# Kernel optimization log

Measured on AMD Instinct MI355X. Metric: run time of the kernel, lower is better.

Reference implementation:

```python
import jax, jax.numpy as jnp
import numpy as np

T, B, H = 2048, 32, 1024
L1, L2, L3 = 100, 10, 1  # cascade 100 -> 10 -> 1 from linear_size=100


def setup_inputs() -> dict:
    key = jax.random.key(0)
    ks = jax.random.split(key, 8)
    def lin_init(k, fan_in, shape):
        # torch nn.Linear default: U(-1/sqrt(fan_in), 1/sqrt(fan_in))
        bound = 1.0 / np.sqrt(fan_in)
        return jax.random.uniform(k, shape, jnp.float32, -bound, bound)
    return {
        "encoder_output": jax.random.normal(ks[0], (T, B, H), jnp.float32),
        "lengths": jax.random.randint(ks[1], (B,), 1, T + 1, jnp.int64),
        "W1": lin_init(ks[2], H, (L1, H)),
        "b1": lin_init(ks[3], H, (L1,)),
        "W2": lin_init(ks[4], L1, (L2, L1)),
        "b2": lin_init(ks[5], L1, (L2,)),
        "W3": lin_init(ks[6], L2, (L3, L2)),
        "b3": lin_init(ks[7], L2, (L3,)),
    }


def reference(encoder_output, lengths, W1, b1, W2, b2, W3, b3):
    # MLP cascade over all timesteps/batch at once: [T,B,H] -> [T,B,1]
    h = jax.nn.relu(jnp.einsum("tbh,lh->tbl", encoder_output, W1) + b1)
    h = jax.nn.relu(jnp.einsum("tbl,ml->tbm", h, W2) + b2)
    logits = jnp.einsum("tbm,om->tbo", h, W3) + b3  # [T,B,1]
    logp = jax.nn.log_sigmoid(logits)[..., 0]       # [T,B]
    # Mask timesteps beyond each sample's length, sum, exponentiate
    mask = jnp.arange(T)[:, None] < lengths[None, :]  # [T,B]
    return jnp.exp(jnp.sum(jnp.where(mask, logp, 0.0), axis=0))  # [B]
```

## Files before the change

kernel.cpp:

```cpp
#include <hip/hip_runtime.h>
#include <stdint.h>


#define T_DIM 2048
#define B_DIM 32
#define H_DIM 1024
#define L1_DIM 100
#define L1_PAD 112
#define L2_DIM 10
#define L2_PAD 16
#define K2_PAD 128
#define NBLK  1024

#define W1B_ELEMS (L1_PAD * H_DIM)
#define W2B_ELEMS (L2_PAD * K2_PAD)
#define PART_OFF_BYTES ((W1B_ELEMS + W2B_ELEMS) * 2)

typedef float v4f __attribute__((ext_vector_type(4)));
typedef short s8  __attribute__((ext_vector_type(8)));

static __device__ __forceinline__ unsigned short f2bf(float f) {
    unsigned int u = __float_as_uint(f);
    u += 0x7fffu + ((u >> 16) & 1u);
    return (unsigned short)(u >> 16);
}

__global__ void convert_weights(const float* __restrict__ W1,
                                const float* __restrict__ W2,
                                unsigned short* __restrict__ wsb) {
    int i = blockIdx.x * 256 + threadIdx.x;
    if (i < W1B_ELEMS) {
        int row = i >> 10, col = i & 1023;
        float v = (row < L1_DIM) ? W1[row * H_DIM + col] : 0.0f;
        wsb[i] = f2bf(v);
    } else {
        int j = i - W1B_ELEMS;
        if (j < W2B_ELEMS) {
            int r = j >> 7, c = j & 127;
            float v = (r < L2_DIM && c < L1_DIM) ? W2[r * L1_DIM + c] : 0.0f;
            wsb[W1B_ELEMS + j] = f2bf(v);
        }
    }
}

__global__ __launch_bounds__(256) void mlp_main(
    const float* __restrict__ enc,
    const int*   __restrict__ lenp,
    const float* __restrict__ b1,
    const float* __restrict__ b2,
    const float* __restrict__ W3,
    const float* __restrict__ b3,
    const unsigned short* __restrict__ w1b,
    const unsigned short* __restrict__ w2b,
    float* __restrict__ partials)
{
    __shared__ __align__(16) unsigned short ldsB[L1_PAD][72];
    __shared__ __align__(16) unsigned short ldsH[64][136];
    __shared__ __align__(16) unsigned short ldsW2[L2_PAD][136];
    __shared__ float ldsPart[2][32];

    const int tid  = threadIdx.x;
    const int blk  = blockIdx.x;
    const int lane = tid & 63;
    const int w    = tid >> 6;
    const int m    = lane & 15;
    const int q    = lane >> 4;

    const bool is64 = (lenp[1] == 0);

    const int tA = 2 * blk + (w >> 1);
    const int bA = ((w & 1) << 4) + m;
    const int lenA = is64 ? lenp[2 * bA] : lenp[bA];
    const bool predA = (tA < lenA);

    int maxlen = 0;
    for (int i = 0; i < B_DIM; ++i) {
        int L = is64 ? lenp[2 * i] : lenp[i];
        maxlen = max(maxlen, L);
    }
    if (2 * blk >= maxlen) {
        if (tid < 32) partials[tid * NBLK + blk] = 0.0f;
        return;
    }

    {
        int r = tid >> 4;
        int c = (tid & 15) << 3;
        *(uint4*)&ldsW2[r][c] = *(const uint4*)(w2b + r * K2_PAD + c);
    }

    float b1v[7];
#pragma unroll
    for (int nt = 0; nt < 7; ++nt) {
        int n = nt * 16 + m;
        b1v[nt] = (n < L1_DIM) ? b1[n] : 0.0f;
    }
    const float b2v = (m < L2_DIM) ? b2[m] : 0.0f;
    const float w3v = (m < L2_DIM) ? W3[m] : 0.0f;
    const float b3s = b3[0];

    const float* aptr = enc + (size_t)(blk * 64 + w * 16 + m) * H_DIM + q * 8;

    v4f acc[7];
#pragma unroll
    for (int nt = 0; nt < 7; ++nt) acc[nt] = (v4f)0.0f;

    for (int kc = 0; kc < 16; ++kc) {
        __syncthreads();
        {
            int base = tid;
#pragma unroll
            for (int it = 0; it < 4; ++it, base += 256) {
                if (it < 3 || base < 896) {
                    int r = base >> 3;
                    int c = (base & 7) << 3;
                    *(uint4*)&ldsB[r][c] =
                        *(const uint4*)(w1b + r * H_DIM + kc * 64 + c);
                }
            }
        }
        __syncthreads();
#pragma unroll
        for (int ks = 0; ks < 2; ++ks) {
            const int k0 = kc * 64 + ks * 32;
            float4 x0, x1;
            if (predA) {
                x0 = *(const float4*)(aptr + k0);
                x1 = *(const float4*)(aptr + k0 + 4);
            } else {
                x0 = make_float4(0.f, 0.f, 0.f, 0.f);
                x1 = make_float4(0.f, 0.f, 0.f, 0.f);
            }
            s8 afrag;
            afrag[0] = (short)f2bf(x0.x); afrag[1] = (short)f2bf(x0.y);
            afrag[2] = (short)f2bf(x0.z); afrag[3] = (short)f2bf(x0.w);
            afrag[4] = (short)f2bf(x1.x); afrag[5] = (short)f2bf(x1.y);
            afrag[6] = (short)f2bf(x1.z); afrag[7] = (short)f2bf(x1.w);
#pragma unroll
            for (int nt = 0; nt < 7; ++nt) {
                s8 bfrag = *(const s8*)&ldsB[nt * 16 + m][ks * 32 + q * 8];
                acc[nt] = __builtin_amdgcn_mfma_f32_16x16x32_bf16(
                    afrag, bfrag, acc[nt], 0, 0, 0);
            }
        }
    }

    __syncthreads();
#pragma unroll
    for (int nt = 0; nt < 7; ++nt) {
#pragma unroll
        for (int reg = 0; reg < 4; ++reg) {
            float h = fmaxf(acc[nt][reg] + b1v[nt], 0.0f);
            ldsH[w * 16 + q * 4 + reg][nt * 16 + m] = f2bf(h);
        }
    }
    {
        int r = tid >> 2;
        int c = 112 + ((tid & 3) << 2);
        *(uint2*)&ldsH[r][c] = make_uint2(0u, 0u);
    }
    __syncthreads();

    v4f acc2 = (v4f)0.0f;
#pragma unroll
    for (int ks = 0; ks < 4; ++ks) {
        s8 a2  = *(const s8*)&ldsH[w * 16 + m][ks * 32 + q * 8];
        s8 b2f = *(const s8*)&ldsW2[m][ks * 32 + q * 8];
        acc2 = __builtin_amdgcn_mfma_f32_16x16x32_bf16(a2, b2f, acc2, 0, 0, 0);
    }

    v4f z;
#pragma unroll
    for (int reg = 0; reg < 4; ++reg) {
        float y2 = fmaxf(acc2[reg] + b2v, 0.0f);
        z[reg] = y2 * w3v;
    }
#pragma unroll
    for (int msk = 1; msk < 16; msk <<= 1) {
#pragma unroll
        for (int reg = 0; reg < 4; ++reg)
            z[reg] += __shfl_xor(z[reg], msk, 16);
    }
    if (m == 0) {
#pragma unroll
        for (int reg = 0; reg < 4; ++reg) {
            int rowLocal = q * 4 + reg;
            int bC = ((w & 1) << 4) + rowLocal;
            int lenC = is64 ? lenp[2 * bC] : lenp[bC];
            float logit = z[reg] + b3s;
            float logp  = fminf(logit, 0.0f) - log1pf(__expf(-fabsf(logit)));
            ldsPart[w >> 1][bC] = (tA < lenC) ? logp : 0.0f;
        }
    }
    __syncthreads();
    if (tid < 32)
        partials[tid * NBLK + blk] = ldsPart[0][tid] + ldsPart[1][tid];
}

__global__ void finalize(const float* __restrict__ partials,
                         float* __restrict__ out) {
    const int b = blockIdx.x;
    const int tid = threadIdx.x;
    float s = 0.0f;
    for (int i = tid; i < NBLK; i += 256) s += partials[b * NBLK + i];
#pragma unroll
    for (int off = 32; off > 0; off >>= 1) s += __shfl_down(s, off, 64);
    __shared__ float red[4];
    if ((tid & 63) == 0) red[tid >> 6] = s;
    __syncthreads();
    if (tid == 0) out[b] = expf(red[0] + red[1] + red[2] + red[3]);
}

extern "C" void kernel_launch(void* const* d_in, const int* in_sizes, int n_in,
                              void* d_out, int out_size, void* d_ws, size_t ws_size,
                              hipStream_t stream) {
    const float* enc = (const float*)d_in[0];
    const int*   len = (const int*)d_in[1];
    const float* W1  = (const float*)d_in[2];
    const float* b1  = (const float*)d_in[3];
    const float* W2  = (const float*)d_in[4];
    const float* b2  = (const float*)d_in[5];
    const float* W3  = (const float*)d_in[6];
    const float* b3  = (const float*)d_in[7];

    unsigned short* wsb = (unsigned short*)d_ws;
    float* partials = (float*)((char*)d_ws + PART_OFF_BYTES);
    float* out = (float*)d_out;

    convert_weights<<<(W1B_ELEMS + W2B_ELEMS + 255) / 256, 256, 0, stream>>>(W1, W2, wsb);
    mlp_main<<<NBLK, 256, 0, stream>>>(enc, len, b1, b2, W3, b3,
                                       wsb, wsb + W1B_ELEMS, partials);
    finalize<<<B_DIM, 256, 0, stream>>>(partials, out);
}
```

Before: 375.5 us.

## Load W1 fragments directly from global and register-prefetch encoder tiles

```diff
diff --git a/kernel.cpp b/kernel.cpp
--- a/kernel.cpp
+++ b/kernel.cpp
@@ -8,12 +8,11 @@
 #define L1_DIM 100
 #define L1_PAD 112
 #define L2_DIM 10
-#define L2_PAD 16
 #define K2_PAD 128
 #define NBLK  1024
 
 #define W1B_ELEMS (L1_PAD * H_DIM)
-#define W2B_ELEMS (L2_PAD * K2_PAD)
+#define W2B_ELEMS (16 * K2_PAD)
 #define PART_OFF_BYTES ((W1B_ELEMS + W2B_ELEMS) * 2)
 
 typedef float v4f __attribute__((ext_vector_type(4)));
@@ -54,9 +53,8 @@
     const unsigned short* __restrict__ w2b,
     float* __restrict__ partials)
 {
-    __shared__ __align__(16) unsigned short ldsB[L1_PAD][72];
     __shared__ __align__(16) unsigned short ldsH[64][136];
-    __shared__ __align__(16) unsigned short ldsW2[L2_PAD][136];
+    __shared__ __align__(16) unsigned short ldsW2[16][136];
     __shared__ float ldsPart[2][32];
 
     const int tid  = threadIdx.x;
@@ -99,53 +97,54 @@
     const float w3v = (m < L2_DIM) ? W3[m] : 0.0f;
     const float b3s = b3[0];
 
-    const float* aptr = enc + (size_t)(blk * 64 + w * 16 + m) * H_DIM + q * 8;
+    const float* ap = enc + (size_t)(blk * 64 + w * 16 + m) * H_DIM + q * 8;
+    const unsigned short* wp = w1b + m * H_DIM + q * 8;
 
     v4f acc[7];
 #pragma unroll
     for (int nt = 0; nt < 7; ++nt) acc[nt] = (v4f)0.0f;
 
+#define LOADA(dst, off)                                                  \
+    do {                                                                 \
+        if (predA) dst = *(const float4*)(ap + (off));                   \
+        else       dst = make_float4(0.f, 0.f, 0.f, 0.f);                \
+    } while (0)
+
+    float4 aP0, aP1, aP2, aP3;
+    LOADA(aP0, 0); LOADA(aP1, 4); LOADA(aP2, 32); LOADA(aP3, 36);
+
+#pragma unroll 4
     for (int kc = 0; kc < 16; ++kc) {
-        __syncthreads();
-        {
-            int base = tid;
-#pragma unroll
-            for (int it = 0; it < 4; ++it, base += 256) {
-                if (it < 3 || base < 896) {
-                    int r = base >> 3;
-                    int c = (base & 7) << 3;
-                    *(uint4*)&ldsB[r][c] =
-                        *(const uint4*)(w1b + r * H_DIM + kc * 64 + c);
-                }
-            }
-        }
-        __syncthreads();
+        float4 aN0, aN1, aN2, aN3;
+        if (kc < 15) {
+            const int o = (kc + 1) * 64;
+            LOADA(aN0, o); LOADA(aN1, o + 4); LOADA(aN2, o + 32); LOADA(aN3, o + 36);
+        } else {
+            aN0 = aN1 = aN2 = aN3 = make_float4(0.f, 0.f, 0.f, 0.f);
+        }
 #pragma unroll
         for (int ks = 0; ks < 2; ++ks) {
-            const int k0 = kc * 64 + ks * 32;
-            float4 x0, x1;
-            if (predA) {
-                x0 = *(const float4*)(aptr + k0);
-                x1 = *(const float4*)(aptr + k0 + 4);
-            } else {
-                x0 = make_float4(0.f, 0.f, 0.f, 0.f);
-                x1 = make_float4(0.f, 0.f, 0.f, 0.f);
-            }
-            s8 afrag;
-            afrag[0] = (short)f2bf(x0.x); afrag[1] = (short)f2bf(x0.y);
-            afrag[2] = (short)f2bf(x0.z); afrag[3] = (short)f2bf(x0.w);
-            afrag[4] = (short)f2bf(x1.x); afrag[5] = (short)f2bf(x1.y);
-            afrag[6] = (short)f2bf(x1.z); afrag[7] = (short)f2bf(x1.w);
-#pragma unroll
-            for (int nt = 0; nt < 7; ++nt) {
-                s8 bfrag = *(const s8*)&ldsB[nt * 16 + m][ks * 32 + q * 8];
+            const unsigned short* wk = wp + kc * 64 + ks * 32;
+            s8 bfr[7];
+#pragma unroll
+            for (int nt = 0; nt < 7; ++nt)
+                bfr[nt] = *(const s8*)(wk + nt * 16 * H_DIM);
+            const float4 x0 = ks ? aP2 : aP0;
+            const float4 x1 = ks ? aP3 : aP1;
+            s8 af;
+            af[0] = (short)f2bf(x0.x); af[1] = (short)f2bf(x0.y);
+            af[2] = (short)f2bf(x0.z); af[3] = (short)f2bf(x0.w);
+            af[4] = (short)f2bf(x1.x); af[5] = (short)f2bf(x1.y);
+            af[6] = (short)f2bf(x1.z); af[7] = (short)f2bf(x1.w);
+#pragma unroll
+            for (int nt = 0; nt < 7; ++nt)
                 acc[nt] = __builtin_amdgcn_mfma_f32_16x16x32_bf16(
-                    afrag, bfrag, acc[nt], 0, 0, 0);
-            }
-        }
-    }
-
-    __syncthreads();
+                    af, bfr[nt], acc[nt], 0, 0, 0);
+        }
+        aP0 = aN0; aP1 = aN1; aP2 = aN2; aP3 = aN3;
+    }
+#undef LOADA
+
 #pragma unroll
     for (int nt = 0; nt < 7; ++nt) {
 #pragma unroll
```

New measurement: 430.1 us. +14.5%, slower.

## Double-buffer W1 tiles via direct global-to-LDS loads, two row tiles per wave

Applied to the files above, without the earlier changes.

```diff
diff --git a/kernel.cpp b/kernel.cpp
--- a/kernel.cpp
+++ b/kernel.cpp
@@ -1,4 +1,5 @@
 #include <hip/hip_runtime.h>
+#include <hip/hip_bf16.h>
 #include <stdint.h>
 
 
@@ -6,15 +7,19 @@
 #define B_DIM 32
 #define H_DIM 1024
 #define L1_DIM 100
-#define L1_PAD 112
 #define L2_DIM 10
-#define L2_PAD 16
 #define K2_PAD 128
-#define NBLK  1024
-
-#define W1B_ELEMS (L1_PAD * H_DIM)
-#define W2B_ELEMS (L2_PAD * K2_PAD)
+#define NPART 512
+
+#define W1B_ELEMS (112 * 1024)
+#define W2B_ELEMS (16 * 128)
 #define PART_OFF_BYTES ((W1B_ELEMS + W2B_ELEMS) * 2)
+
+#define CHUNK_BYTES 14336
+#define LDSH_OFF    0
+#define LDSW2_OFF   34816
+#define LDSPART_OFF 39168
+#define LDS_TOTAL   39680
 
 typedef float v4f __attribute__((ext_vector_type(4)));
 typedef short s8  __attribute__((ext_vector_type(8)));
@@ -23,6 +28,15 @@
     unsigned int u = __float_as_uint(f);
     u += 0x7fffu + ((u >> 16) & 1u);
     return (unsigned short)(u >> 16);
+}
+
+static __device__ __forceinline__ s8 pack8(float4 a, float4 b) {
+    union { s8 v; __hip_bfloat162 h[4]; } u;
+    u.h[0] = __float22bfloat162_rn(make_float2(a.x, a.y));
+    u.h[1] = __float22bfloat162_rn(make_float2(a.z, a.w));
+    u.h[2] = __float22bfloat162_rn(make_float2(b.x, b.y));
+    u.h[3] = __float22bfloat162_rn(make_float2(b.z, b.w));
+    return u.v;
 }
 
 __global__ void convert_weights(const float* __restrict__ W1,
@@ -54,10 +68,7 @@
     const unsigned short* __restrict__ w2b,
     float* __restrict__ partials)
 {
-    __shared__ __align__(16) unsigned short ldsB[L1_PAD][72];
-    __shared__ __align__(16) unsigned short ldsH[64][136];
-    __shared__ __align__(16) unsigned short ldsW2[L2_PAD][136];
-    __shared__ float ldsPart[2][32];
+    __shared__ __align__(16) unsigned char smem[LDS_TOTAL];
 
     const int tid  = threadIdx.x;
     const int blk  = blockIdx.x;
@@ -68,25 +79,27 @@
 
     const bool is64 = (lenp[1] == 0);
 
-    const int tA = 2 * blk + (w >> 1);
-    const int bA = ((w & 1) << 4) + m;
-    const int lenA = is64 ? lenp[2 * bA] : lenp[bA];
-    const bool predA = (tA < lenA);
-
     int maxlen = 0;
     for (int i = 0; i < B_DIM; ++i) {
         int L = is64 ? lenp[2 * i] : lenp[i];
         maxlen = max(maxlen, L);
     }
-    if (2 * blk >= maxlen) {
-        if (tid < 32) partials[tid * NBLK + blk] = 0.0f;
+    if (4 * blk >= maxlen) {
+        if (tid < 32) partials[tid * NPART + blk] = 0.0f;
         return;
     }
 
+    const int t = 4 * blk + w;
+    const int len0 = is64 ? lenp[2 * m] : lenp[m];
+    const int len1 = is64 ? lenp[2 * (16 + m)] : lenp[16 + m];
+    const bool pred0 = (t < len0);
+    const bool pred1 = (t < len1);
+    const bool waveActive = (t < maxlen);
+
     {
-        int r = tid >> 4;
-        int c = (tid & 15) << 3;
-        *(uint4*)&ldsW2[r][c] = *(const uint4*)(w2b + r * K2_PAD + c);
+        unsigned short* ldsW2 = (unsigned short*)(smem + LDSW2_OFF);
+        int r = tid >> 4, c = (tid & 15) << 3;
+        *(uint4*)(ldsW2 + r * 136 + c) = *(const uint4*)(w2b + r * K2_PAD + c);
     }
 
     float b1v[7];
@@ -99,102 +112,153 @@
     const float w3v = (m < L2_DIM) ? W3[m] : 0.0f;
     const float b3s = b3[0];
 
-    const float* aptr = enc + (size_t)(blk * 64 + w * 16 + m) * H_DIM + q * 8;
-
-    v4f acc[7];
-#pragma unroll
-    for (int nt = 0; nt < 7; ++nt) acc[nt] = (v4f)0.0f;
-
-    for (int kc = 0; kc < 16; ++kc) {
-        __syncthreads();
-        {
-            int base = tid;
-#pragma unroll
-            for (int it = 0; it < 4; ++it, base += 256) {
-                if (it < 3 || base < 896) {
-                    int r = base >> 3;
-                    int c = (base & 7) << 3;
-                    *(uint4*)&ldsB[r][c] =
-                        *(const uint4*)(w1b + r * H_DIM + kc * 64 + c);
-                }
+    const float* ap0 = enc + (size_t)(blk * 128 + w * 32 + m) * H_DIM + q * 8;
+    const float* ap1 = ap0 + 16 * H_DIM;
+    const int fragoff = lane * 16;
+
+    v4f acc0[7], acc1[7];
+#pragma unroll
+    for (int nt = 0; nt < 7; ++nt) { acc0[nt] = (v4f)0.0f; acc1[nt] = (v4f)0.0f; }
+
+#define STAGE(kc, BASE)                                                        \
+    {                                                                          \
+        _Pragma("unroll")                                                      \
+        for (int it = 0; it < 4; ++it) {                                       \
+            int j = it * 256 + tid;                                            \
+            if (it < 3 || tid < 128) {                                         \
+                int rest = j >> 6;                           \
+                int ks = (rest >= 7) ? 1 : 0;                                  \
+                int nt = rest - ks * 7;                                        \
+                const unsigned short* g = w1b + (nt * 16 + (j & 15)) * H_DIM + \
+                                          (kc) * 64 + ks * 32 + ((j >> 4) & 3) * 8; \
+                __builtin_amdgcn_global_load_lds(                              \
+                    (const __attribute__((address_space(1))) unsigned int*)g,  \
+                    (__attribute__((address_space(3))) unsigned int*)           \
+                        (smem + (BASE) + (j & ~63) * 16),                      \
+                    16, 0, 0);                                                 \
+            }                                                                  \
+        }                                                                      \
+    }
+
+#define KBODY(kc, RD, WR)                                                      \
+    {                                                                          \
+        if ((kc) < 15) STAGE((kc) + 1, WR);                                    \
+        if (waveActive) {                                                      \
+            const int kb = (kc) * 64;                                          \
+            const float4 z4 = make_float4(0.f, 0.f, 0.f, 0.f);                 \
+            float4 a00 = pred0 ? *(const float4*)(ap0 + kb)      : z4;         \
+            float4 a01 = pred0 ? *(const float4*)(ap0 + kb + 4)  : z4;         \
+            float4 a02 = pred0 ? *(const float4*)(ap0 + kb + 32) : z4;         \
+            float4 a03 = pred0 ? *(const float4*)(ap0 + kb + 36) : z4;         \
+            float4 a10 = pred1 ? *(const float4*)(ap1 + kb)      : z4;         \
+            float4 a11 = pred1 ? *(const float4*)(ap1 + kb + 4)  : z4;         \
+            float4 a12 = pred1 ? *(const float4*)(ap1 + kb + 32) : z4;         \
+            float4 a13 = pred1 ? *(const float4*)(ap1 + kb + 36) : z4;         \
+            s8 af0 = pack8(a00, a01);                                          \
+            s8 af1 = pack8(a10, a11);                                          \
+            _Pragma("unroll")                                                  \
+            for (int nt = 0; nt < 7; ++nt) {                                   \
+                s8 bf = *(const s8*)(smem + (RD) + nt * 1024 + fragoff);       \
+                acc0[nt] = __builtin_amdgcn_mfma_f32_16x16x32_bf16(af0, bf, acc0[nt], 0, 0, 0); \
+                acc1[nt] = __builtin_amdgcn_mfma_f32_16x16x32_bf16(af1, bf, acc1[nt], 0, 0, 0); \
+            }                                                                  \
+            af0 = pack8(a02, a03);                                             \
+            af1 = pack8(a12, a13);                                             \
+            _Pragma("unroll")                                                  \
+            for (int nt = 0; nt < 7; ++nt) {                                   \
+                s8 bf = *(const s8*)(smem + (RD) + (7 + nt) * 1024 + fragoff); \
+                acc0[nt] = __builtin_amdgcn_mfma_f32_16x16x32_bf16(af0, bf, acc0[nt], 0, 0, 0); \
+                acc1[nt] = __builtin_amdgcn_mfma_f32_16x16x32_bf16(af1, bf, acc1[nt], 0, 0, 0); \
+            }                                                                  \
+        }                                                                      \
+        __syncthreads();                                                       \
+    }
+
+    STAGE(0, 0)
+    __syncthreads();
+
+    KBODY(0, 0, CHUNK_BYTES)
+    KBODY(1, CHUNK_BYTES, 0)
+    KBODY(2, 0, CHUNK_BYTES)
+    KBODY(3, CHUNK_BYTES, 0)
+    KBODY(4, 0, CHUNK_BYTES)
+    KBODY(5, CHUNK_BYTES, 0)
+    KBODY(6, 0, CHUNK_BYTES)
+    KBODY(7, CHUNK_BYTES, 0)
+    KBODY(8, 0, CHUNK_BYTES)
+    KBODY(9, CHUNK_BYTES, 0)
+    KBODY(10, 0, CHUNK_BYTES)
+    KBODY(11, CHUNK_BYTES, 0)
+    KBODY(12, 0, CHUNK_BYTES)
+    KBODY(13, CHUNK_BYTES, 0)
+    KBODY(14, 0, CHUNK_BYTES)
+    KBODY(15, CHUNK_BYTES, 0)
+
+#undef KBODY
+#undef STAGE
+
+    unsigned short* ldsH = (unsigned short*)(smem + LDSH_OFF);
+#pragma unroll
+    for (int f = 0; f < 2; ++f) {
+#pragma unroll
+        for (int nt = 0; nt < 7; ++nt) {
+#pragma unroll
+            for (int reg = 0; reg < 4; ++reg) {
+                int row = w * 32 + f * 16 + q * 4 + reg;
+                int col = nt * 16 + m;
+                float a = f ? acc1[nt][reg] : acc0[nt][reg];
+                ldsH[row * 136 + col] = f2bf(fmaxf(a + b1v[nt], 0.0f));
             }
         }
-        __syncthreads();
-#pragma unroll
-        for (int ks = 0; ks < 2; ++ks) {
-            const int k0 = kc * 64 + ks * 32;
-            float4 x0, x1;
-            if (predA) {
-                x0 = *(const float4*)(aptr + k0);
-                x1 = *(const float4*)(aptr + k0 + 4);
-            } else {
-                x0 = make_float4(0.f, 0.f, 0.f, 0.f);
-                x1 = make_float4(0.f, 0.f, 0.f, 0.f);
+    }
+    {
+        int r = tid >> 1, c = 112 + (tid & 1) * 8;
+        uint4 z; z.x = z.y = z.z = z.w = 0u;
+        *(uint4*)(ldsH + r * 136 + c) = z;
+    }
+    __syncthreads();
+
+    unsigned short* ldsW2 = (unsigned short*)(smem + LDSW2_OFF);
+    v4f acc2[2];
+    acc2[0] = (v4f)0.0f; acc2[1] = (v4f)0.0f;
+#pragma unroll
+    for (int ks2 = 0; ks2 < 4; ++ks2) {
+        s8 bw = *(const s8*)(ldsW2 + m * 136 + ks2 * 32 + q * 8);
+#pragma unroll
+        for (int f = 0; f < 2; ++f) {
+            s8 ah = *(const s8*)(ldsH + (w * 32 + f * 16 + m) * 136 + ks2 * 32 + q * 8);
+            acc2[f] = __builtin_amdgcn_mfma_f32_16x16x32_bf16(ah, bw, acc2[f], 0, 0, 0);
+        }
+    }
+
+    float* ldsPart = (float*)(smem + LDSPART_OFF);
+#pragma unroll
+    for (int f = 0; f < 2; ++f) {
+        v4f zv;
+#pragma unroll
+        for (int reg = 0; reg < 4; ++reg)
+            zv[reg] = fmaxf(acc2[f][reg] + b2v, 0.0f) * w3v;
+#pragma unroll
+        for (int msk = 1; msk < 16; msk <<= 1) {
+#pragma unroll
+            for (int reg = 0; reg < 4; ++reg)
+                zv[reg] += __shfl_xor(zv[reg], msk, 16);
+        }
+        if (m == 0) {
+#pragma unroll
+            for (int reg = 0; reg < 4; ++reg) {
+                int b = f * 16 + q * 4 + reg;
+                int lenB = is64 ? lenp[2 * b] : lenp[b];
+                float logit = zv[reg] + b3s;
+                float logp  = fminf(logit, 0.0f) - log1pf(__expf(-fabsf(logit)));
+                ldsPart[w * 32 + b] = (t < lenB) ? logp : 0.0f;
             }
-            s8 afrag;
-            afrag[0] = (short)f2bf(x0.x); afrag[1] = (short)f2bf(x0.y);
-            afrag[2] = (short)f2bf(x0.z); afrag[3] = (short)f2bf(x0.w);
-            afrag[4] = (short)f2bf(x1.x); afrag[5] = (short)f2bf(x1.y);
-            afrag[6] = (short)f2bf(x1.z); afrag[7] = (short)f2bf(x1.w);
-#pragma unroll
-            for (int nt = 0; nt < 7; ++nt) {
-                s8 bfrag = *(const s8*)&ldsB[nt * 16 + m][ks * 32 + q * 8];
-                acc[nt] = __builtin_amdgcn_mfma_f32_16x16x32_bf16(
-                    afrag, bfrag, acc[nt], 0, 0, 0);
-            }
-        }
-    }
-
-    __syncthreads();
-#pragma unroll
-    for (int nt = 0; nt < 7; ++nt) {
-#pragma unroll
-        for (int reg = 0; reg < 4; ++reg) {
-            float h = fmaxf(acc[nt][reg] + b1v[nt], 0.0f);
-            ldsH[w * 16 + q * 4 + reg][nt * 16 + m] = f2bf(h);
-        }
-    }
-    {
-        int r = tid >> 2;
-        int c = 112 + ((tid & 3) << 2);
-        *(uint2*)&ldsH[r][c] = make_uint2(0u, 0u);
-    }
-    __syncthreads();
-
-    v4f acc2 = (v4f)0.0f;
-#pragma unroll
-    for (int ks = 0; ks < 4; ++ks) {
-        s8 a2  = *(const s8*)&ldsH[w * 16 + m][ks * 32 + q * 8];
-        s8 b2f = *(const s8*)&ldsW2[m][ks * 32 + q * 8];
-        acc2 = __builtin_amdgcn_mfma_f32_16x16x32_bf16(a2, b2f, acc2, 0, 0, 0);
-    }
-
-    v4f z;
-#pragma unroll
-    for (int reg = 0; reg < 4; ++reg) {
-        float y2 = fmaxf(acc2[reg] + b2v, 0.0f);
-        z[reg] = y2 * w3v;
-    }
-#pragma unroll
-    for (int msk = 1; msk < 16; msk <<= 1) {
-#pragma unroll
-        for (int reg = 0; reg < 4; ++reg)
-            z[reg] += __shfl_xor(z[reg], msk, 16);
-    }
-    if (m == 0) {
-#pragma unroll
-        for (int reg = 0; reg < 4; ++reg) {
-            int rowLocal = q * 4 + reg;
-            int bC = ((w & 1) << 4) + rowLocal;
-            int lenC = is64 ? lenp[2 * bC] : lenp[bC];
-            float logit = z[reg] + b3s;
-            float logp  = fminf(logit, 0.0f) - log1pf(__expf(-fabsf(logit)));
-            ldsPart[w >> 1][bC] = (tA < lenC) ? logp : 0.0f;
         }
     }
     __syncthreads();
     if (tid < 32)
-        partials[tid * NBLK + blk] = ldsPart[0][tid] + ldsPart[1][tid];
+        partials[tid * NPART + blk] =
+            (ldsPart[tid] + ldsPart[32 + tid]) + (ldsPart[64 + tid] + ldsPart[96 + tid]);
 }
 
 __global__ void finalize(const float* __restrict__ partials,
@@ -202,7 +266,7 @@
     const int b = blockIdx.x;
     const int tid = threadIdx.x;
     float s = 0.0f;
-    for (int i = tid; i < NBLK; i += 256) s += partials[b * NBLK + i];
+    for (int i = tid; i < NPART; i += 256) s += partials[b * NPART + i];
 #pragma unroll
     for (int off = 32; off > 0; off >>= 1) s += __shfl_down(s, off, 64);
     __shared__ float red[4];
@@ -228,7 +292,7 @@
     float* out = (float*)d_out;
 
     convert_weights<<<(W1B_ELEMS + W2B_ELEMS + 255) / 256, 256, 0, stream>>>(W1, W2, wsb);
-    mlp_main<<<NBLK, 256, 0, stream>>>(enc, len, b1, b2, W3, b3,
-                                       wsb, wsb + W1B_ELEMS, partials);
+    mlp_main<<<NPART, 256, 0, stream>>>(enc, len, b1, b2, W3, b3,
+                                        wsb, wsb + W1B_ELEMS, partials);
     finalize<<<B_DIM, 256, 0, stream>>>(partials, out);
 }
```

After: 445.9 us. 18.7% more time.
